# Kernel tuning notes

Hardware: AMD Instinct MI355X
Metric: run time of the kernel (lower is better)

The kernel has to match this reference:

```python
import jax, jax.numpy as jnp
import numpy as np

NEG_SLOPE = 0.2  # PyG GATConv default


def gat_layer(x, src, dst, W, a_src, a_dst, b, heads, ch, num_nodes):
    # x: [N, F_in]; W: [F_in, heads*ch]; a_src/a_dst: [heads, ch]; b: [heads*ch]
    h = (x @ W).reshape(num_nodes, heads, ch)                      # [N,H,C]
    al_s = jnp.einsum('nhc,hc->nh', h, a_src)                      # [N,H]
    al_d = jnp.einsum('nhc,hc->nh', h, a_dst)                      # [N,H]
    e = jax.nn.leaky_relu(al_s[src] + al_d[dst], NEG_SLOPE)        # [E,H]
    # segment softmax over incoming edges of each destination node
    emax = jax.ops.segment_max(e, dst, num_segments=num_nodes)     # [N,H]
    ee = jnp.exp(e - emax[dst])
    denom = jax.ops.segment_sum(ee, dst, num_segments=num_nodes)   # [N,H]
    alpha = ee / denom[dst]                                        # [E,H]
    msg = h[src] * alpha[..., None]                                # [E,H,C]
    out = jax.ops.segment_sum(msg, dst, num_segments=num_nodes)    # [N,H,C]
    return out.reshape(num_nodes, heads * ch) + b


def setup_inputs() -> dict:
    key = jax.random.key(0)
    ks = jax.random.split(key, 12)
    N, F_in, H1, C1, OUT = 50000, 128, 6, 32, 2
    E = 800000
    x = jax.random.normal(ks[0], (N, F_in), dtype=jnp.float32)
    edge_index = jax.random.randint(ks[1], (2, E), 0, N, dtype=jnp.int64)
    s = 0.1
    return {
        'x': x,
        'edge_index': edge_index,
        'W1': jax.random.normal(ks[2], (F_in, H1 * C1), dtype=jnp.float32) * s,
        'a1_src': jax.random.normal(ks[3], (H1, C1), dtype=jnp.float32) * s,
        'a1_dst': jax.random.normal(ks[4], (H1, C1), dtype=jnp.float32) * s,
        'b1': jnp.zeros((H1 * C1,), dtype=jnp.float32),
        'W2': jax.random.normal(ks[5], (H1 * C1, 1 * OUT), dtype=jnp.float32) * s,
        'a2_src': jax.random.normal(ks[6], (1, OUT), dtype=jnp.float32) * s,
        'a2_dst': jax.random.normal(ks[7], (1, OUT), dtype=jnp.float32) * s,
        'b2': jnp.zeros((OUT,), dtype=jnp.float32),
    }


def reference(x, edge_index, W1, a1_src, a1_dst, b1, W2, a2_src, a2_dst, b2):
    N = x.shape[0]
    loop = jnp.arange(N, dtype=edge_index.dtype)
    src = jnp.concatenate([edge_index[0], loop])  # add_self_loops=True (PyG default)
    dst = jnp.concatenate([edge_index[1], loop])
    h = gat_layer(x, src, dst, W1, a1_src, a1_dst, b1, heads=6, ch=32, num_nodes=N)
    h = jax.nn.relu(h)
    h = gat_layer(h, src, dst, W2, a2_src, a2_dst, b2, heads=1, ch=2, num_nodes=N)
    return jax.nn.log_softmax(h, axis=1)
```

## Files before the change

kernel.cpp:

```cpp
#include <hip/hip_runtime.h>
#include <hip/hip_fp16.h>

#define LRELU(v) ((v) > 0.0f ? (v) : 0.2f * (v))

constexpr int F_IN = 128;
constexpr int NH1  = 6;
constexpr int D1   = 192;

typedef _Float16 half8 __attribute__((ext_vector_type(8)));
typedef float floatx4 __attribute__((ext_vector_type(4)));

__device__ __forceinline__ void wave_lds_fence() {
  __builtin_amdgcn_wave_barrier();
  asm volatile("s_waitcnt lgkmcnt(0)" ::: "memory");
  __builtin_amdgcn_wave_barrier();
}

__global__ __launch_bounds__(256) void k_hist(const float* __restrict__ W1,
                                              __half* __restrict__ w1t,
                                              const int* __restrict__ dst,
                                              int* __restrict__ cnt,
                                              int* __restrict__ pose, int E) {
  int tid = blockIdx.x * 256 + threadIdx.x;
  if (tid < F_IN * D1) {
    int k = tid / D1, n = tid - k * D1;
    w1t[(size_t)n * F_IN + k] = __float2half(W1[tid]);
  }
  if (tid < E) {
    pose[tid] = atomicAdd(&cnt[dst[tid]], 1);
  }
}

__global__ __launch_bounds__(256) void k_gemm1(const float* __restrict__ x,
                                               const __half* __restrict__ w1t,
                                               const float* __restrict__ a1s,
                                               const float* __restrict__ a1d,
                                               __half* __restrict__ h1h,
                                               float* __restrict__ als,
                                               float* __restrict__ ald, int N) {
  int wv = blockIdx.x * 4 + (threadIdx.x >> 6);
  int m0 = wv * 16;
  if (m0 >= N) return;
  int lane = threadIdx.x & 63;
  int ln15 = lane & 15, q = lane >> 4;

  float avs[12], avd[12];
#pragma unroll
  for (int f = 0; f < 12; ++f) {
    int idx = (f >> 1) * 32 + (f & 1) * 16 + ln15;
    avs[f] = a1s[idx];
    avd[f] = a1d[idx];
  }

  floatx4 acc[12];
#pragma unroll
  for (int f = 0; f < 12; ++f) acc[f] = (floatx4){0.f, 0.f, 0.f, 0.f};

  int arowi = m0 + ln15;
  if (arowi >= N) arowi = N - 1;
  const float* arow = x + (size_t)arowi * F_IN + q * 8;
#pragma unroll
  for (int kc = 0; kc < F_IN; kc += 32) {
    float4 u0 = *(const float4*)(arow + kc);
    float4 u1 = *(const float4*)(arow + kc + 4);
    half8 a;
    a[0] = (_Float16)u0.x; a[1] = (_Float16)u0.y; a[2] = (_Float16)u0.z; a[3] = (_Float16)u0.w;
    a[4] = (_Float16)u1.x; a[5] = (_Float16)u1.y; a[6] = (_Float16)u1.z; a[7] = (_Float16)u1.w;
#pragma unroll
    for (int f = 0; f < 12; ++f) {
      half8 b = *(const half8*)(w1t + (size_t)(16 * f + ln15) * F_IN + kc + q * 8);
      acc[f] = __builtin_amdgcn_mfma_f32_16x16x32_f16(a, b, acc[f], 0, 0, 0);
    }
  }

#pragma unroll
  for (int f = 0; f < 12; ++f) {
#pragma unroll
    for (int r = 0; r < 4; ++r) {
      int n = m0 + q * 4 + r;
      if (n < N) h1h[(size_t)n * D1 + 16 * f + ln15] = __float2half(acc[f][r]);
    }
  }

#pragma unroll
  for (int r = 0; r < 4; ++r) {
    float ps[6] = {0.f, 0.f, 0.f, 0.f, 0.f, 0.f};
    float pd[6] = {0.f, 0.f, 0.f, 0.f, 0.f, 0.f};
#pragma unroll
    for (int f = 0; f < 12; ++f) {
      ps[f >> 1] = fmaf(acc[f][r], avs[f], ps[f >> 1]);
      pd[f >> 1] = fmaf(acc[f][r], avd[f], pd[f >> 1]);
    }
#pragma unroll
    for (int h = 0; h < 6; ++h) {
#pragma unroll
      for (int m = 8; m; m >>= 1) {
        ps[h] += __shfl_xor(ps[h], m);
        pd[h] += __shfl_xor(pd[h], m);
      }
    }
    float os = 0.f, od = 0.f;
#pragma unroll
    for (int h = 0; h < 6; ++h)
      if (ln15 == h) { os = ps[h]; od = pd[h]; }
    int n = m0 + q * 4 + r;
    if (ln15 < 6 && n < N) {
      als[(size_t)n * 6 + ln15] = os;
      ald[(size_t)n * 6 + ln15] = od;
    }
  }
}

__global__ void k_scan1(const int* __restrict__ cnt, int* __restrict__ offs,
                        int* __restrict__ bsum, int N) {
  int t = threadIdx.x;
  int idx = blockIdx.x * 256 + t;
  int lane = t & 63, w = t >> 6;
  int v = (idx < N) ? cnt[idx] : 0;
  int incl = v;
#pragma unroll
  for (int d = 1; d < 64; d <<= 1) {
    int u = __shfl_up(incl, d);
    if (lane >= d) incl += u;
  }
  __shared__ int wt[4];
  if (lane == 63) wt[w] = incl;
  __syncthreads();
  int woff = 0;
  for (int i = 0; i < w; ++i) woff += wt[i];
  if (idx < N) offs[idx] = woff + incl - v;
  if (t == 255) bsum[blockIdx.x] = woff + incl;
}

__global__ void k_scan2(int* __restrict__ bsum, int* __restrict__ boff, int NB) {
  int t = threadIdx.x;
  int lane = t & 63, w = t >> 6;
  int v = (t < NB) ? bsum[t] : 0;
  int incl = v;
#pragma unroll
  for (int d = 1; d < 64; d <<= 1) {
    int u = __shfl_up(incl, d);
    if (lane >= d) incl += u;
  }
  __shared__ int wt[4];
  if (lane == 63) wt[w] = incl;
  __syncthreads();
  int woff = 0;
  for (int i = 0; i < w; ++i) woff += wt[i];
  if (t < NB) boff[t] = woff + incl - v;
}

__global__ void k_scan3(int* __restrict__ offs, const int* __restrict__ boff,
                        const int* __restrict__ bsum, int N, int NB) {
  int idx = blockIdx.x * 256 + threadIdx.x;
  if (idx < N) offs[idx] += boff[blockIdx.x];
  if (idx == 0) offs[N] = boff[NB - 1] + bsum[NB - 1];
}

__global__ __launch_bounds__(256) void k_place(const int* __restrict__ src,
                                               const int* __restrict__ dst,
                                               const int* __restrict__ offs,
                                               const int* __restrict__ pose,
                                               int* __restrict__ ssort, int E) {
  int e = blockIdx.x * 256 + threadIdx.x;
  if (e < E) {
    ssort[offs[dst[e]] + pose[e]] = src[e];
  }
}

__global__ __launch_bounds__(256) void k_agg1(
    const __half* __restrict__ h1h, const float* __restrict__ als, const float* __restrict__ ald,
    const int* __restrict__ offs, const int* __restrict__ srcs,
    const float* __restrict__ b1, const float* __restrict__ W2,
    const float* __restrict__ a2s, const float* __restrict__ a2d,
    float* __restrict__ h2, float* __restrict__ al2s, float* __restrict__ al2d, int N) {
  __shared__ float wbuf[4][64][9];
  int wid = threadIdx.x >> 6, lane = threadIdx.x & 63;
  int d = blockIdx.x * 4 + wid;
  if (d >= N) return;
  int off = offs[d], cnt = offs[d + 1] - off;
  int tot = cnt + 1;

  float aldh[6];
  {
    const float* ap = ald + (size_t)d * 6;
    float2 q0 = *(const float2*)ap, q1 = *(const float2*)(ap + 2), q2 = *(const float2*)(ap + 4);
    aldh[0] = q0.x; aldh[1] = q0.y; aldh[2] = q1.x;
    aldh[3] = q1.y; aldh[4] = q2.x; aldh[5] = q2.y;
  }

  float dh[6] = {0.f, 0.f, 0.f, 0.f, 0.f, 0.f};
  int nchunk = (tot + 63) >> 6;

  float a0 = 0.f, a1 = 0.f, a2 = 0.f;
  const int hw = lane >> 4;
  const int hh = 4 + (lane >> 5);

  auto body = [&](int j) {
    float w_a = wbuf[wid][j][hw];
    float w_b = wbuf[wid][j][hh];
    int s = __float_as_int(wbuf[wid][j][6]);
    const __half* hp = h1h + (size_t)s * D1;
    float2 v = __half22float2(*(const __half2*)(hp + 2 * lane));
    float vh = __half2float(hp[128 + lane]);
    a0 = fmaf(w_a, v.x, a0);
    a1 = fmaf(w_a, v.y, a1);
    a2 = fmaf(w_b, vh, a2);
  };
  auto jloop = [&](int jmax) {
    int j = 0;
    for (; j + 3 < jmax; j += 4) { body(j); body(j + 1); body(j + 2); body(j + 3); }
    for (; j < jmax; ++j) body(j);
  };

  if (nchunk == 1) {
    float wreg[6];
    int sreg = 0;
    if (lane < tot) {
      int s = (lane == cnt) ? d : srcs[off + lane];
      sreg = s;
      const float* ap = als + (size_t)s * 6;
      float2 p0 = *(const float2*)ap, p1 = *(const float2*)(ap + 2), p2 = *(const float2*)(ap + 4);
      float ev[6] = {p0.x, p0.y, p1.x, p1.y, p2.x, p2.y};
#pragma unroll
      for (int h = 0; h < 6; ++h) {
        float e = ev[h] + aldh[h];
        e = LRELU(e);
        wreg[h] = __expf(e);
        dh[h] = wreg[h];
      }
    }
#pragma unroll
    for (int h = 0; h < 6; ++h) {
#pragma unroll
      for (int m = 32; m; m >>= 1) dh[h] += __shfl_xor(dh[h], m);
      dh[h] = 1.0f / dh[h];
    }
    if (lane < tot) {
#pragma unroll
      for (int h = 0; h < 6; ++h) wbuf[wid][lane][h] = wreg[h] * dh[h];
      wbuf[wid][lane][6] = __int_as_float(sreg);
    }
    wave_lds_fence();
    jloop(tot);
  } else {
    for (int c = 0; c < nchunk; ++c) {
      int i = c * 64 + lane;
      if (i < tot) {
        int s = (i == cnt) ? d : srcs[off + i];
        const float* ap = als + (size_t)s * 6;
        float2 p0 = *(const float2*)ap, p1 = *(const float2*)(ap + 2), p2 = *(const float2*)(ap + 4);
        float ev[6] = {p0.x, p0.y, p1.x, p1.y, p2.x, p2.y};
#pragma unroll
        for (int h = 0; h < 6; ++h) {
          float e = ev[h] + aldh[h];
          e = LRELU(e);
          dh[h] += __expf(e);
        }
      }
    }
#pragma unroll
    for (int h = 0; h < 6; ++h) {
#pragma unroll
      for (int m = 32; m; m >>= 1) dh[h] += __shfl_xor(dh[h], m);
      dh[h] = 1.0f / dh[h];
    }
    for (int c = 0; c < nchunk; ++c) {
      int i = c * 64 + lane;
      if (i < tot) {
        int s = (i == cnt) ? d : srcs[off + i];
        const float* ap = als + (size_t)s * 6;
        float2 p0 = *(const float2*)ap, p1 = *(const float2*)(ap + 2), p2 = *(const float2*)(ap + 4);
        float ev[6] = {p0.x, p0.y, p1.x, p1.y, p2.x, p2.y};
#pragma unroll
        for (int h = 0; h < 6; ++h) {
          float e = ev[h] + aldh[h];
          e = LRELU(e);
          wbuf[wid][lane][h] = __expf(e) * dh[h];
        }
        wbuf[wid][lane][6] = __int_as_float(s);
      }
      wave_lds_fence();
      int jmax = tot - c * 64;
      if (jmax > 64) jmax = 64;
      jloop(jmax);
      wave_lds_fence();
    }
  }

  float2 bv = *(const float2*)(b1 + 2 * lane);
  float v0 = fmaxf(a0 + bv.x, 0.f);
  float v1 = fmaxf(a1 + bv.y, 0.f);
  float v2 = fmaxf(a2 + b1[128 + lane], 0.f);
  float4 ww = *(const float4*)(W2 + 4 * lane);
  float2 wh = *(const float2*)(W2 + (128 + lane) * 2);
  float s0 = v0 * ww.x + v1 * ww.z + v2 * wh.x;
  float s1 = v0 * ww.y + v1 * ww.w + v2 * wh.y;
#pragma unroll
  for (int m = 32; m; m >>= 1) {
    s0 += __shfl_xor(s0, m);
    s1 += __shfl_xor(s1, m);
  }
  if (lane == 0) {
    h2[d * 2] = s0;
    h2[d * 2 + 1] = s1;
    al2s[d] = s0 * a2s[0] + s1 * a2s[1];
    al2d[d] = s0 * a2d[0] + s1 * a2d[1];
  }
}

__global__ __launch_bounds__(256) void k_agg2(
    const float* __restrict__ h2, const float* __restrict__ al2s,
    const float* __restrict__ al2d, const int* __restrict__ offs,
    const int* __restrict__ srcs, const float* __restrict__ b2,
    float* __restrict__ out, int N) {
  int tid = blockIdx.x * 256 + threadIdx.x;
  int g = tid >> 3, r = tid & 7;
  if (g >= N) return;
  int off = offs[g], cnt = offs[g + 1] - off;
  int tot = cnt + 1;
  float ad = al2d[g];
  float den = 0.f, o0 = 0.f, o1 = 0.f;
  for (int i = r; i < tot; i += 8) {
    int s = (i == cnt) ? g : srcs[off + i];
    float e = al2s[s] + ad;
    e = LRELU(e);
    float a = __expf(e);
    float2 hv = *(const float2*)(h2 + (size_t)s * 2);
    den += a;
    o0 = fmaf(a, hv.x, o0);
    o1 = fmaf(a, hv.y, o1);
  }
#pragma unroll
  for (int m = 4; m; m >>= 1) {
    den += __shfl_xor(den, m);
    o0 += __shfl_xor(o0, m);
    o1 += __shfl_xor(o1, m);
  }
  if (r == 0) {
    float inv = 1.0f / den;
    o0 = o0 * inv + b2[0];
    o1 = o1 * inv + b2[1];
    float mm = fmaxf(o0, o1);
    float l = mm + logf(__expf(o0 - mm) + __expf(o1 - mm));
    *(float2*)(out + (size_t)g * 2) = make_float2(o0 - l, o1 - l);
  }
}

extern "C" void kernel_launch(void* const* d_in, const int* in_sizes, int n_in,
                              void* d_out, int out_size, void* d_ws, size_t ws_size,
                              hipStream_t stream) {
  const float* x   = (const float*)d_in[0];
  const int*   ei  = (const int*)d_in[1];
  const float* W1  = (const float*)d_in[2];
  const float* a1s = (const float*)d_in[3];
  const float* a1d = (const float*)d_in[4];
  const float* b1  = (const float*)d_in[5];
  const float* W2  = (const float*)d_in[6];
  const float* a2s = (const float*)d_in[7];
  const float* a2d = (const float*)d_in[8];
  const float* b2  = (const float*)d_in[9];
  float* out = (float*)d_out;

  const int N = in_sizes[0] / F_IN;
  const int E = in_sizes[1] / 2;
  const int* srcp = ei;
  const int* dstp = ei + E;

  char* w = (char*)d_ws;
  auto alloc = [&](size_t bytes) {
    char* p = w;
    w += (bytes + 255) & ~(size_t)255;
    return p;
  };
  __half* h1h   = (__half*)alloc((size_t)N * D1 * 2);
  __half* w1t   = (__half*)alloc((size_t)F_IN * D1 * 2);
  float* als    = (float*)alloc((size_t)N * NH1 * 4);
  float* ald    = (float*)alloc((size_t)N * NH1 * 4);
  float* h2     = (float*)alloc((size_t)N * 2 * 4);
  float* al2s   = (float*)alloc((size_t)N * 4);
  float* al2d   = (float*)alloc((size_t)N * 4);
  int*   cnt    = (int*)alloc((size_t)N * 4);
  int*   offs   = (int*)alloc((size_t)(N + 1) * 4);
  int*   pose   = (int*)alloc((size_t)E * 4);
  int*   bsum   = (int*)alloc(1024);
  int*   boff   = (int*)alloc(1024);
  int*   ssort  = (int*)alloc((size_t)E * 4);

  const int NB = (N + 255) / 256;

  hipMemsetAsync(cnt, 0, (size_t)N * 4, stream);

  k_hist<<<(E + 255) / 256, 256, 0, stream>>>(W1, w1t, dstp, cnt, pose, E);

  int nwave = (N + 15) / 16;
  k_gemm1<<<(nwave + 3) / 4, 256, 0, stream>>>(x, w1t, a1s, a1d, h1h, als, ald, N);

  k_scan1<<<NB, 256, 0, stream>>>(cnt, offs, bsum, N);
  k_scan2<<<1, 256, 0, stream>>>(bsum, boff, NB);
  k_scan3<<<NB, 256, 0, stream>>>(offs, boff, bsum, N, NB);
  k_place<<<(E + 255) / 256, 256, 0, stream>>>(srcp, dstp, offs, pose, ssort, E);

  k_agg1<<<(N + 3) / 4, 256, 0, stream>>>(h1h, als, ald, offs, ssort, b1, W2,
                                          a2s, a2d, h2, al2s, al2d, N);
  k_agg2<<<(N * 8 + 255) / 256, 256, 0, stream>>>(h2, al2s, al2d, offs, ssort, b2, out, N);
}
```

Measured before the change: 238.9 us.

## Shard degree-count atomics into 8 slices and pack layer-2 node data

The edge histogram now spreads its atomics across 8 per-block-group copies of the count array, cutting contention on the same destination counter. The scan folds the 8 slices into per-slice prefixes that the placement kernel uses. The layer-2 features and attention logits are packed into one float4 per node, so each gather in the second aggregation is a single 16-byte load. The aggregation loop also stores byte offsets in LDS to save a multiply. The cost is a larger memset and scan over 8N counts plus an extra spre array read during placement.

```diff
diff --git a/kernel.cpp b/kernel.cpp
--- a/kernel.cpp
+++ b/kernel.cpp
@@ -20,14 +20,15 @@
                                               __half* __restrict__ w1t,
                                               const int* __restrict__ dst,
                                               int* __restrict__ cnt,
-                                              int* __restrict__ pose, int E) {
+                                              int* __restrict__ pose, int N, int E) {
   int tid = blockIdx.x * 256 + threadIdx.x;
   if (tid < F_IN * D1) {
     int k = tid / D1, n = tid - k * D1;
     w1t[(size_t)n * F_IN + k] = __float2half(W1[tid]);
   }
   if (tid < E) {
-    pose[tid] = atomicAdd(&cnt[dst[tid]], 1);
+    int s = blockIdx.x & 7;
+    pose[tid] = atomicAdd(&cnt[s * N + dst[tid]], 1);
   }
 }
 
@@ -111,12 +112,19 @@
   }
 }
 
-__global__ void k_scan1(const int* __restrict__ cnt, int* __restrict__ offs,
-                        int* __restrict__ bsum, int N) {
+__global__ void k_scanA(const int* __restrict__ cnt, int* __restrict__ spre,
+                        int* __restrict__ offs, int* __restrict__ bsum, int N) {
   int t = threadIdx.x;
   int idx = blockIdx.x * 256 + t;
   int lane = t & 63, w = t >> 6;
-  int v = (idx < N) ? cnt[idx] : 0;
+  int run = 0;
+#pragma unroll
+  for (int s = 0; s < 8; ++s) {
+    int c = (idx < N) ? cnt[s * N + idx] : 0;
+    if (idx < N) spre[s * N + idx] = run;
+    run += c;
+  }
+  int v = run;
   int incl = v;
 #pragma unroll
   for (int d = 1; d < 64; d <<= 1) {
@@ -132,7 +140,7 @@
   if (t == 255) bsum[blockIdx.x] = woff + incl;
 }
 
-__global__ void k_scan2(int* __restrict__ bsum, int* __restrict__ boff, int NB) {
+__global__ void k_scanB(int* __restrict__ bsum, int* __restrict__ boff, int NB) {
   int t = threadIdx.x;
   int lane = t & 63, w = t >> 6;
   int v = (t < NB) ? bsum[t] : 0;
@@ -150,7 +158,7 @@
   if (t < NB) boff[t] = woff + incl - v;
 }
 
-__global__ void k_scan3(int* __restrict__ offs, const int* __restrict__ boff,
+__global__ void k_scanC(int* __restrict__ offs, const int* __restrict__ boff,
                         const int* __restrict__ bsum, int N, int NB) {
   int idx = blockIdx.x * 256 + threadIdx.x;
   if (idx < N) offs[idx] += boff[blockIdx.x];
@@ -160,11 +168,14 @@
 __global__ __launch_bounds__(256) void k_place(const int* __restrict__ src,
                                                const int* __restrict__ dst,
                                                const int* __restrict__ offs,
+                                               const int* __restrict__ spre,
                                                const int* __restrict__ pose,
-                                               int* __restrict__ ssort, int E) {
+                                               int* __restrict__ ssort, int N, int E) {
   int e = blockIdx.x * 256 + threadIdx.x;
   if (e < E) {
-    ssort[offs[dst[e]] + pose[e]] = src[e];
+    int d = dst[e];
+    int s = (e >> 8) & 7;
+    ssort[offs[d] + spre[s * N + d] + pose[e]] = src[e];
   }
 }
 
@@ -173,7 +184,7 @@
     const int* __restrict__ offs, const int* __restrict__ srcs,
     const float* __restrict__ b1, const float* __restrict__ W2,
     const float* __restrict__ a2s, const float* __restrict__ a2d,
-    float* __restrict__ h2, float* __restrict__ al2s, float* __restrict__ al2d, int N) {
+    float4* __restrict__ pk, int N) {
   __shared__ float wbuf[4][64][9];
   int wid = threadIdx.x >> 6, lane = threadIdx.x & 63;
   int d = blockIdx.x * 4 + wid;
@@ -199,8 +210,8 @@
   auto body = [&](int j) {
     float w_a = wbuf[wid][j][hw];
     float w_b = wbuf[wid][j][hh];
-    int s = __float_as_int(wbuf[wid][j][6]);
-    const __half* hp = h1h + (size_t)s * D1;
+    int soff = __float_as_int(wbuf[wid][j][6]);
+    const __half* hp = (const __half*)((const char*)h1h + soff);
     float2 v = __half22float2(*(const __half2*)(hp + 2 * lane));
     float vh = __half2float(hp[128 + lane]);
     a0 = fmaf(w_a, v.x, a0);
@@ -239,7 +250,7 @@
     if (lane < tot) {
 #pragma unroll
       for (int h = 0; h < 6; ++h) wbuf[wid][lane][h] = wreg[h] * dh[h];
-      wbuf[wid][lane][6] = __int_as_float(sreg);
+      wbuf[wid][lane][6] = __int_as_float(sreg * (D1 * 2));
     }
     wave_lds_fence();
     jloop(tot);
@@ -278,7 +289,7 @@
           e = LRELU(e);
           wbuf[wid][lane][h] = __expf(e) * dh[h];
         }
-        wbuf[wid][lane][6] = __int_as_float(s);
+        wbuf[wid][lane][6] = __int_as_float(s * (D1 * 2));
       }
       wave_lds_fence();
       int jmax = tot - c * 64;
@@ -302,16 +313,14 @@
     s1 += __shfl_xor(s1, m);
   }
   if (lane == 0) {
-    h2[d * 2] = s0;
-    h2[d * 2 + 1] = s1;
-    al2s[d] = s0 * a2s[0] + s1 * a2s[1];
-    al2d[d] = s0 * a2d[0] + s1 * a2d[1];
+    pk[d] = make_float4(s0, s1,
+                        s0 * a2s[0] + s1 * a2s[1],
+                        s0 * a2d[0] + s1 * a2d[1]);
   }
 }
 
 __global__ __launch_bounds__(256) void k_agg2(
-    const float* __restrict__ h2, const float* __restrict__ al2s,
-    const float* __restrict__ al2d, const int* __restrict__ offs,
+    const float4* __restrict__ pk, const int* __restrict__ offs,
     const int* __restrict__ srcs, const float* __restrict__ b2,
     float* __restrict__ out, int N) {
   int tid = blockIdx.x * 256 + threadIdx.x;
@@ -319,17 +328,17 @@
   if (g >= N) return;
   int off = offs[g], cnt = offs[g + 1] - off;
   int tot = cnt + 1;
-  float ad = al2d[g];
+  float ad = pk[g].w;
   float den = 0.f, o0 = 0.f, o1 = 0.f;
   for (int i = r; i < tot; i += 8) {
     int s = (i == cnt) ? g : srcs[off + i];
-    float e = al2s[s] + ad;
+    float4 p = pk[s];
+    float e = p.z + ad;
     e = LRELU(e);
     float a = __expf(e);
-    float2 hv = *(const float2*)(h2 + (size_t)s * 2);
     den += a;
-    o0 = fmaf(a, hv.x, o0);
-    o1 = fmaf(a, hv.y, o1);
+    o0 = fmaf(a, p.x, o0);
+    o1 = fmaf(a, p.y, o1);
   }
 #pragma unroll
   for (int m = 4; m; m >>= 1) {
@@ -377,10 +386,9 @@
   __half* w1t   = (__half*)alloc((size_t)F_IN * D1 * 2);
   float* als    = (float*)alloc((size_t)N * NH1 * 4);
   float* ald    = (float*)alloc((size_t)N * NH1 * 4);
-  float* h2     = (float*)alloc((size_t)N * 2 * 4);
-  float* al2s   = (float*)alloc((size_t)N * 4);
-  float* al2d   = (float*)alloc((size_t)N * 4);
-  int*   cnt    = (int*)alloc((size_t)N * 4);
+  float4* pk    = (float4*)alloc((size_t)N * 16);
+  int*   cnt    = (int*)alloc((size_t)N * 8 * 4);
+  int*   spre   = (int*)alloc((size_t)N * 8 * 4);
   int*   offs   = (int*)alloc((size_t)(N + 1) * 4);
   int*   pose   = (int*)alloc((size_t)E * 4);
   int*   bsum   = (int*)alloc(1024);
@@ -389,19 +397,19 @@
 
   const int NB = (N + 255) / 256;
 
-  hipMemsetAsync(cnt, 0, (size_t)N * 4, stream);
-
-  k_hist<<<(E + 255) / 256, 256, 0, stream>>>(W1, w1t, dstp, cnt, pose, E);
+  hipMemsetAsync(cnt, 0, (size_t)N * 8 * 4, stream);
+
+  k_hist<<<(E + 255) / 256, 256, 0, stream>>>(W1, w1t, dstp, cnt, pose, N, E);
 
   int nwave = (N + 15) / 16;
   k_gemm1<<<(nwave + 3) / 4, 256, 0, stream>>>(x, w1t, a1s, a1d, h1h, als, ald, N);
 
-  k_scan1<<<NB, 256, 0, stream>>>(cnt, offs, bsum, N);
-  k_scan2<<<1, 256, 0, stream>>>(bsum, boff, NB);
-  k_scan3<<<NB, 256, 0, stream>>>(offs, boff, bsum, N, NB);
-  k_place<<<(E + 255) / 256, 256, 0, stream>>>(srcp, dstp, offs, pose, ssort, E);
+  k_scanA<<<NB, 256, 0, stream>>>(cnt, spre, offs, bsum, N);
+  k_scanB<<<1, 256, 0, stream>>>(bsum, boff, NB);
+  k_scanC<<<NB, 256, 0, stream>>>(offs, boff, bsum, N, NB);
+  k_place<<<(E + 255) / 256, 256, 0, stream>>>(srcp, dstp, offs, spre, pose, ssort, N, E);
 
   k_agg1<<<(N + 3) / 4, 256, 0, stream>>>(h1h, als, ald, offs, ssort, b1, W2,
-                                          a2s, a2d, h2, al2s, al2d, N);
-  k_agg2<<<(N * 8 + 255) / 256, 256, 0, stream>>>(h2, al2s, al2d, offs, ssort, b2, out, N);
-}
+                                          a2s, a2d, pk, N);
+  k_agg2<<<(N * 8 + 255) / 256, 256, 0, stream>>>(pk, offs, ssort, b2, out, N);
+}
```

Measured after the change: 237.7 us. About the same (-0.5%).
